# Performance work log

Hardware: AMD Instinct MI355X
Metric: run time of the kernel (lower is better)

Reference implementation:

```python
import jax, jax.numpy as jnp
import numpy as np

B, S, D_MODEL, D_K, D_V = 8, 2048, 1024, 1024, 1024


def setup_inputs() -> dict:
    key = jax.random.key(0)
    ks = jax.random.split(key, 10)
    scale = 1.0 / np.sqrt(D_MODEL)
    return {
        "inputs_q": jax.random.normal(ks[0], (B, S, D_MODEL), dtype=jnp.float32),
        "inputs_k": jax.random.normal(ks[1], (B, S, D_MODEL), dtype=jnp.float32),
        "inputs_v": jax.random.normal(ks[2], (B, S, D_MODEL), dtype=jnp.float32),
        "mask": jax.random.randint(ks[3], (B, S), 0, 2, dtype=jnp.int32),
        "Wq": jax.random.normal(ks[4], (D_MODEL, D_K), dtype=jnp.float32) * scale,
        "bq": jnp.zeros((D_K,), dtype=jnp.float32),
        "Wk": jax.random.normal(ks[5], (D_MODEL, D_K), dtype=jnp.float32) * scale,
        "bk": jnp.zeros((D_K,), dtype=jnp.float32),
        "Wv": jax.random.normal(ks[6], (D_MODEL, D_V), dtype=jnp.float32) * scale,
        "bv": jnp.zeros((D_V,), dtype=jnp.float32),
    }


def reference(inputs_q, inputs_k, inputs_v, mask, Wq, bq, Wk, bk, Wv, bv):
    # Dense projections: [B,S,d_model] @ [d_model,d] + bias
    q = jnp.einsum("bsd,dk->bsk", inputs_q, Wq) + bq
    k = jnp.einsum("bsd,dk->bsk", inputs_k, Wk) + bk
    v = jnp.einsum("bsd,dv->bsv", inputs_v, Wv) + bv
    # scaled dot-product scores [B,S,S]
    scores = jnp.einsum("bqk,bsk->bqs", q, k) / jnp.sqrt(jnp.float32(D_K))
    # padding mask [B,S] -> matrix mask via min(row, col); 1 = valid
    m = mask.astype(jnp.float32)
    matrix_mask = jnp.minimum(m[:, :, None], m[:, None, :])  # [B,S,S]
    mask_float = 1.0 - matrix_mask  # 1 where masked
    scores = scores + mask_float * (-1e9)
    attention_weights = jax.nn.softmax(scores, axis=-1)
    out = jnp.einsum("bqs,bsv->bqv", attention_weights, v)  # [B,S,d_v]
    return out
```

## Files before the change

### kernel.cpp

```cpp
#include <hip/hip_runtime.h>
#include <stdint.h>


typedef unsigned short u16;
typedef __attribute__((ext_vector_type(8))) short short8;
typedef __attribute__((ext_vector_type(4))) float f32x4;

__device__ __forceinline__ u16 f2bf(float x) {
  unsigned u = __float_as_uint(x);
  return (u16)((u + 0x7FFFu + ((u >> 16) & 1u)) >> 16);
}
__device__ __forceinline__ float bf2f(u16 h) {
  return __uint_as_float(((unsigned)h) << 16);
}

__device__ __forceinline__ void stage16(const void* g, void* l) {
  const __attribute__((address_space(1))) uint32_t* gp =
      (const __attribute__((address_space(1))) uint32_t*)(uintptr_t)g;
  __attribute__((address_space(3))) uint32_t* lp =
      (__attribute__((address_space(3))) uint32_t*)(uintptr_t)l;
  __builtin_amdgcn_global_load_lds(gp, lp, 16, 0, 0);
}

__device__ __forceinline__ short8 ld8(const char* p, int off) {
  return *(const short8*)(p + off);
}

__global__ __launch_bounds__(256) void maskscan(const int* __restrict__ mask,
                                                int* __restrict__ idxA,
                                                int* __restrict__ nvA,
                                                int* __restrict__ nvpadA) {
  const int b = blockIdx.x;
  const int t = threadIdx.x, lane = t & 63, w = t >> 6;
  const int* m = mask + b * 2048;
  int v[8], loc = 0;
#pragma unroll
  for (int i = 0; i < 8; ++i) { v[i] = m[t * 8 + i]; loc += v[i]; }
  int sc = loc;
  for (int off = 1; off < 64; off <<= 1) {
    int n = __shfl_up(sc, off);
    if (lane >= off) sc += n;
  }
  __shared__ int wsum[4];
  if (lane == 63) wsum[w] = sc;
  __syncthreads();
  int woff = 0;
  for (int i = 0; i < w; ++i) woff += wsum[i];
  int pos = woff + sc - loc;
#pragma unroll
  for (int i = 0; i < 8; ++i)
    if (v[i]) idxA[b * 2048 + (pos++)] = t * 8 + i;
  if (t == 255) {
    const int nv = woff + sc;
    nvA[b] = nv;
    nvpadA[b] = (nv + 255) & ~255;
  }
}

__global__ __launch_bounds__(256) void compact3(const float* __restrict__ Xq,
                                                const float* __restrict__ Xk,
                                                const float* __restrict__ Xv,
                                                const int* __restrict__ idxA,
                                                const int* __restrict__ nvA,
                                                u16* __restrict__ Oq,
                                                u16* __restrict__ Ok,
                                                u16* __restrict__ Ov) {
  const int b = blockIdx.y, j = blockIdx.x, z = blockIdx.z;
  if (j >= nvA[b]) return;
  const float* X = (z == 0) ? Xq : (z == 1) ? Xk : Xv;
  u16* out = (z == 0) ? Oq : (z == 1) ? Ok : Ov;
  const int src = idxA[b * 2048 + j];
  const float4* s = (const float4*)(X + ((size_t)b * 2048 + src) * 1024);
  ushort4* d = (ushort4*)(out + ((size_t)b * 2048 + j) * 1024);
  const float4 f = s[threadIdx.x];
  ushort4 o;
  o.x = f2bf(f.x); o.y = f2bf(f.y); o.z = f2bf(f.z); o.w = f2bf(f.w);
  d[threadIdx.x] = o;
}

__global__ __launch_bounds__(256) void colpart(const float* __restrict__ X,
                                               float* __restrict__ partial) {
  const int b = blockIdx.x, dq = blockIdx.y, sck = blockIdx.z;
  const int d = dq * 256 + threadIdx.x;
  const float* p = X + ((size_t)b * 2048 + sck * 256) * 1024 + d;
  float s0 = 0, s1 = 0, s2 = 0, s3 = 0;
  for (int r = 0; r < 256; r += 4) {
    s0 += p[(size_t)(r + 0) * 1024];
    s1 += p[(size_t)(r + 1) * 1024];
    s2 += p[(size_t)(r + 2) * 1024];
    s3 += p[(size_t)(r + 3) * 1024];
  }
  partial[((size_t)b * 8 + sck) * 1024 + d] = (s0 + s1) + (s2 + s3);
}

__global__ __launch_bounds__(256) void vpartk(const float* __restrict__ partial,
                                              const float* __restrict__ Wv,
                                              float* __restrict__ vpart) {
  const int b = blockIdx.x, cq = blockIdx.y, dk = blockIdx.z;
  const int t = threadIdx.x;
  __shared__ float mx[128];
  if (t < 128) {
    const int d = dk * 128 + t;
    float m = 0;
#pragma unroll
    for (int i = 0; i < 8; ++i) m += partial[((size_t)b * 8 + i) * 1024 + d];
    mx[t] = m * (1.0f / 2048.0f);
  }
  __syncthreads();
  const int c = cq * 256 + t;
  const float* wp = Wv + (size_t)(dk * 128) * 1024 + c;
  float acc = 0;
#pragma unroll 4
  for (int i = 0; i < 128; ++i) acc += mx[i] * wp[(size_t)i * 1024];
  vpart[((size_t)b * 8 + dk) * 1024 + c] = acc;
}

__global__ __launch_bounds__(256) void vmeanred(const float* __restrict__ vpart,
                                                const float* __restrict__ bv,
                                                float* __restrict__ vmean) {
  const int b = blockIdx.x;
  const int c = blockIdx.y * 256 + threadIdx.x;
  float acc = bv[c];
#pragma unroll
  for (int i = 0; i < 8; ++i) acc += vpart[((size_t)b * 8 + i) * 1024 + c];
  vmean[b * 1024 + c] = acc;
}

__global__ __launch_bounds__(256) void bcast(const int* __restrict__ mask,
                                             const float* __restrict__ vmean,
                                             float* __restrict__ out) {
  const int b = blockIdx.y, row = blockIdx.x;
  if (mask[b * 2048 + row] != 0) return;
  const float4 vv = ((const float4*)(vmean + b * 1024))[threadIdx.x];
  ((float4*)(out + ((size_t)b * 2048 + row) * 1024))[threadIdx.x] = vv;
}

__global__ __launch_bounds__(256) void wtrans3(const float* __restrict__ Wq,
                                               const float* __restrict__ Wk,
                                               const float* __restrict__ Wv,
                                               u16* __restrict__ WT) {
  __shared__ float tile[32][33];
  const int z = blockIdx.z;
  const float* W = (z == 0) ? Wq : (z == 1) ? Wk : Wv;
  u16* out = WT + (size_t)z * 1024 * 1024;
  const int tx = threadIdx.x, ty = threadIdx.y;
  const int d0 = blockIdx.y * 32, n0 = blockIdx.x * 32;
#pragma unroll
  for (int i = 0; i < 4; ++i)
    tile[ty + 8 * i][tx] = W[(size_t)(d0 + ty + 8 * i) * 1024 + n0 + tx];
  __syncthreads();
#pragma unroll
  for (int i = 0; i < 4; ++i)
    out[(size_t)(n0 + ty + 8 * i) * 1024 + d0 + tx] = f2bf(tile[tx][ty + 8 * i]);
}


#define BAR __builtin_amdgcn_s_barrier()
#define SB __builtin_amdgcn_sched_barrier(0)
#define LGK0 asm volatile("s_waitcnt lgkmcnt(0)" ::: "memory")
#define VM4 asm volatile("s_waitcnt vmcnt(4)" ::: "memory")
#define VM0 asm volatile("s_waitcnt vmcnt(0)" ::: "memory")

#define RDA4(P0, P1, MH)                                      \
  {                                                           \
    _Pragma("unroll") for (int mf_ = 0; mf_ < 4; ++mf_) {     \
      afr[0][mf_] = ld8(P0, (MH) * 8192 + mf_ * 2048);        \
      afr[1][mf_] = ld8(P1, (MH) * 8192 + mf_ * 2048);        \
    }                                                         \
  }

#define RDB2(DST, P0, P1, NH)                                 \
  {                                                           \
    DST[0][0] = ld8(P0, (NH) * 4096);                         \
    DST[0][1] = ld8(P0, (NH) * 4096 + 2048);                  \
    DST[1][0] = ld8(P1, (NH) * 4096);                         \
    DST[1][1] = ld8(P1, (NH) * 4096 + 2048);                  \
  }

#define MQ16(ACC, NH, BF)                                                \
  __builtin_amdgcn_s_setprio(1);                                         \
  {                                                                      \
    _Pragma("unroll") for (int ks_ = 0; ks_ < 2; ++ks_)                  \
        _Pragma("unroll") for (int mf_ = 0; mf_ < 4; ++mf_)              \
            _Pragma("unroll") for (int nf_ = 0; nf_ < 2; ++nf_)          \
                ACC[mf_][(NH) * 2 + nf_] =                               \
                    __builtin_amdgcn_mfma_f32_16x16x32_bf16(             \
                        afr[ks_][mf_], BF[ks_][nf_],                     \
                        ACC[mf_][(NH) * 2 + nf_], 0, 0, 0);              \
  }                                                                      \
  __builtin_amdgcn_s_setprio(0);

template <int MODE>
__global__ __launch_bounds__(512, 2) void gemm8p(
    const u16* __restrict__ A, const u16* __restrict__ B,
    void* __restrict__ C, void* __restrict__ C1, void* __restrict__ C2,
    const float* __restrict__ b0, const float* __restrict__ b1,
    const float* __restrict__ b2,
    const int* __restrict__ nvpadA, const int* __restrict__ nvA,
    const int* __restrict__ idxA,
    int K, int lda, int ldb, int ldc,
    size_t Az, size_t Bz, size_t Cz) {
  __shared__ __attribute__((aligned(16))) char smem[131072];
  const int tid = threadIdx.x;
  const int lane = tid & 63;
  const int w = tid >> 6;
  const int wr = w >> 2;
  const int wc = w & 3;

  const int bx = blockIdx.x;
  const int z = bx & 7;
  int r = bx >> 3;
  int bm, bn, o = 0;
  if constexpr (MODE == 0) { o = r >> 5; r &= 31; bm = r >> 2; bn = r & 3; }
  else if constexpr (MODE == 2) { bm = r >> 3; bn = r & 7; }
  else { bm = r >> 2; bn = r & 3; }

  const int nvp = nvpadA[z];
  if (bm * 256 >= nvp) return;
  if constexpr (MODE == 2) { if (bn * 256 >= nvp) return; }

  const u16* Ap = A;
  const u16* Bp = B;
  if constexpr (MODE == 0) {
    Ap += (size_t)o * (8u * 2048u * 1024u) + (size_t)z * (2048u * 1024u);
    Bp += (size_t)o * (1024u * 1024u);
  } else {
    Ap += (size_t)z * Az;
    Bp += (size_t)z * Bz;
  }
  const int Kz = (MODE == 3) ? nvp : K;
  const int half = Kz >> 7;

  const int srow = w * 8 + (lane >> 3);
  const int scol = ((lane & 7) ^ (lane >> 3)) << 3;
  const u16* Ab0 = Ap + (size_t)(bm * 256 + srow) * lda + scol;
  const u16* Ab1 = Ab0 + (size_t)64 * lda;
  const u16* Ab2 = Ab0 + (size_t)128 * lda;
  const u16* Ab3 = Ab0 + (size_t)192 * lda;
  const u16* Bb0 = Bp + (size_t)(bn * 256 + srow) * ldb + scol;
  const u16* Bb1 = Bb0 + (size_t)64 * ldb;
  const u16* Bb2 = Bb0 + (size_t)128 * ldb;
  const u16* Bb3 = Bb0 + (size_t)192 * ldb;
  char* ldsW = smem + w * 1024;

  const int fr = lane & 15;
  const int fq = lane >> 4;
  const int fx = (fr & 7) << 4;
  const char* pak0 = smem + wr * 16384 + fr * 128 + ((fq * 16) ^ fx);
  const char* pak1 = smem + wr * 16384 + fr * 128 + ((64 + fq * 16) ^ fx);
  const char* pak0b = pak0 + 65536;
  const char* pak1b = pak1 + 65536;
  const char* pbk0 = smem + 32768 + wc * 8192 + fr * 128 + ((fq * 16) ^ fx);
  const char* pbk1 = smem + 32768 + wc * 8192 + fr * 128 + ((64 + fq * 16) ^ fx);
  const char* pbk0b = pbk0 + 65536;
  const char* pbk1b = pbk1 + 65536;

  f32x4 acc0[4][4] = {};
  f32x4 acc1[4][4] = {};
  short8 afr[2][4], bf0[2][2], bf1[2][2];

  stage16(Bb0, ldsW + 32768); stage16(Bb1, ldsW + 40960);
  stage16(Bb2, ldsW + 49152); stage16(Bb3, ldsW + 57344);
  stage16(Ab0, ldsW + 0);     stage16(Ab1, ldsW + 8192);
  stage16(Ab2, ldsW + 16384); stage16(Ab3, ldsW + 24576);
  stage16(Bb0 + 64, ldsW + 98304);  stage16(Bb1 + 64, ldsW + 106496);
  stage16(Bb2 + 64, ldsW + 114688); stage16(Bb3 + 64, ldsW + 122880);
  VM4;
  BAR;

  int koff = 0;
  for (int i = 0; i < half - 1; ++i) {
    const int o1 = koff + 64, o2 = koff + 128, o3 = koff + 192;
    RDA4(pak0, pak1, 0); RDB2(bf0, pbk0, pbk1, 0);
    stage16(Ab0 + o1, ldsW + 65536); stage16(Ab1 + o1, ldsW + 73728);
    SB; BAR; LGK0; MQ16(acc0, 0, bf0); BAR;
    RDB2(bf1, pbk0, pbk1, 1);
    stage16(Ab2 + o1, ldsW + 81920); stage16(Ab3 + o1, ldsW + 90112);
    SB; BAR; LGK0; MQ16(acc0, 1, bf1); BAR;
    RDA4(pak0, pak1, 1);
    stage16(Bb0 + o2, ldsW + 32768); stage16(Bb1 + o2, ldsW + 40960);
    SB; BAR; LGK0; MQ16(acc1, 0, bf0); BAR;
    stage16(Bb2 + o2, ldsW + 49152); stage16(Bb3 + o2, ldsW + 57344);
    SB; BAR; MQ16(acc1, 1, bf1); VM4; BAR;
    RDA4(pak0b, pak1b, 0); RDB2(bf0, pbk0b, pbk1b, 0);
    stage16(Ab0 + o2, ldsW + 0); stage16(Ab1 + o2, ldsW + 8192);
    SB; BAR; LGK0; MQ16(acc0, 0, bf0); BAR;
    RDB2(bf1, pbk0b, pbk1b, 1);
    stage16(Ab2 + o2, ldsW + 16384); stage16(Ab3 + o2, ldsW + 24576);
    SB; BAR; LGK0; MQ16(acc0, 1, bf1); BAR;
    RDA4(pak0b, pak1b, 1);
    stage16(Bb0 + o3, ldsW + 98304); stage16(Bb1 + o3, ldsW + 106496);
    SB; BAR; LGK0; MQ16(acc1, 0, bf0); BAR;
    stage16(Bb2 + o3, ldsW + 114688); stage16(Bb3 + o3, ldsW + 122880);
    SB; BAR; MQ16(acc1, 1, bf1); VM4; BAR;
    koff += 128;
  }
  {
    const int o1 = koff + 64;
    RDA4(pak0, pak1, 0); RDB2(bf0, pbk0, pbk1, 0);
    stage16(Ab0 + o1, ldsW + 65536); stage16(Ab1 + o1, ldsW + 73728);
    SB; BAR; LGK0; MQ16(acc0, 0, bf0); BAR;
    RDB2(bf1, pbk0, pbk1, 1);
    stage16(Ab2 + o1, ldsW + 81920); stage16(Ab3 + o1, ldsW + 90112);
    SB; BAR; LGK0; MQ16(acc0, 1, bf1); BAR;
    RDA4(pak0, pak1, 1);
    SB; BAR; LGK0; MQ16(acc1, 0, bf0); BAR;
    SB; BAR; MQ16(acc1, 1, bf1); VM0; BAR;
    RDA4(pak0b, pak1b, 0); RDB2(bf0, pbk0b, pbk1b, 0);
    SB; BAR; LGK0; MQ16(acc0, 0, bf0); BAR;
    RDB2(bf1, pbk0b, pbk1b, 1);
    SB; BAR; LGK0; MQ16(acc0, 1, bf1); BAR;
    RDA4(pak0b, pak1b, 1);
    SB; BAR; LGK0; MQ16(acc1, 0, bf0); BAR;
    SB; BAR; MQ16(acc1, 1, bf1); BAR;
  }

  const int colb = bn * 256 + wc * 64 + fr;
#pragma unroll
  for (int mh = 0; mh < 2; ++mh) {
    f32x4(&ac)[4][4] = mh ? acc1 : acc0;
    const int rowl = bm * 256 + wr * 128 + mh * 64 + fq * 4;
    if constexpr (MODE == 0) {
      if (o < 2) {
        const float* bp = o ? b1 : b0;
        u16* Cb = (u16*)(o ? C1 : C) + (size_t)z * (2048u * 1024u);
#pragma unroll
        for (int mf = 0; mf < 4; ++mf)
#pragma unroll
          for (int n = 0; n < 4; ++n) {
            const int c = colb + n * 16;
            const float bv = bp[c];
#pragma unroll
            for (int j = 0; j < 4; ++j)
              Cb[(size_t)(rowl + mf * 16 + j) * 1024 + c] =
                  f2bf(ac[mf][n][j] + bv);
          }
      } else {
        u16* Cb = (u16*)C2;
#pragma unroll
        for (int mf = 0; mf < 4; ++mf) {
          const int s_ = rowl + mf * 16;
#pragma unroll
          for (int n = 0; n < 4; ++n) {
            const int c = colb + n * 16;
            const float bv = b2[c];
            ushort4 ov;
            ov.x = f2bf(ac[mf][n][0] + bv);
            ov.y = f2bf(ac[mf][n][1] + bv);
            ov.z = f2bf(ac[mf][n][2] + bv);
            ov.w = f2bf(ac[mf][n][3] + bv);
            *(ushort4*)&Cb[((size_t)z * 1024 + c) * 2048 + s_] = ov;
          }
        }
      }
    } else if constexpr (MODE == 2) {
      u16* Cb = (u16*)C + (size_t)z * Cz;
#pragma unroll
      for (int mf = 0; mf < 4; ++mf)
#pragma unroll
        for (int n = 0; n < 4; ++n) {
          const int c = colb + n * 16;
#pragma unroll
          for (int j = 0; j < 4; ++j)
            Cb[(size_t)(rowl + mf * 16 + j) * ldc + c] =
                f2bf(ac[mf][n][j] * 0.03125f);
        }
    } else {
      const int nv = nvA[z];
      const int* idxp = idxA + z * 2048;
      float* Ob = (float*)C;
#pragma unroll
      for (int mf = 0; mf < 4; ++mf)
#pragma unroll
        for (int j = 0; j < 4; ++j) {
          const int rowc = rowl + mf * 16 + j;
          if (rowc < nv) {
            const int gr = idxp[rowc];
            float* orow = Ob + ((size_t)z * 2048 + gr) * 1024;
#pragma unroll
            for (int n = 0; n < 4; ++n) orow[colb + n * 16] = ac[mf][n][j];
          }
        }
    }
  }
}

__global__ __launch_bounds__(256) void softmaxc(u16* __restrict__ scores,
                                                const int* __restrict__ nvA,
                                                const int* __restrict__ nvpadA) {
  const int b = blockIdx.y, row = blockIdx.x;
  const int nv = nvA[b];
  if (row >= nv) return;
  const int nvp = nvpadA[b];
  const int t = threadIdx.x, lane = t & 63, w = t >> 6;
  u16* sc = scores + ((size_t)b * 2048 + row) * 2048;
  const int c0 = t * 8;
  float v[8];
  if (c0 < nvp) {
    const ushort4 h0 = *(const ushort4*)&sc[c0];
    const ushort4 h1 = *(const ushort4*)&sc[c0 + 4];
    v[0] = bf2f(h0.x); v[1] = bf2f(h0.y); v[2] = bf2f(h0.z); v[3] = bf2f(h0.w);
    v[4] = bf2f(h1.x); v[5] = bf2f(h1.y); v[6] = bf2f(h1.z); v[7] = bf2f(h1.w);
  } else {
#pragma unroll
    for (int i = 0; i < 8; ++i) v[i] = 0.f;
  }
  float lmax = -3.0e38f;
#pragma unroll
  for (int i = 0; i < 8; ++i)
    if (c0 + i < nv) lmax = fmaxf(lmax, v[i]);
#pragma unroll
  for (int off = 32; off >= 1; off >>= 1) lmax = fmaxf(lmax, __shfl_xor(lmax, off));
  __shared__ float red[8];
  if (lane == 0) red[w] = lmax;
  __syncthreads();
  const float bmax = fmaxf(fmaxf(red[0], red[1]), fmaxf(red[2], red[3]));
  float e[8];
  float lsum = 0.f;
#pragma unroll
  for (int i = 0; i < 8; ++i) {
    e[i] = (c0 + i < nv) ? __expf(v[i] - bmax) : 0.f;
    lsum += e[i];
  }
#pragma unroll
  for (int off = 32; off >= 1; off >>= 1) lsum += __shfl_xor(lsum, off);
  if (lane == 0) red[4 + w] = lsum;
  __syncthreads();
  const float inv = 1.0f / ((red[4] + red[5]) + (red[6] + red[7]));
  if (c0 < nvp) {
    ushort4 o0, o1;
    o0.x = f2bf(e[0] * inv); o0.y = f2bf(e[1] * inv);
    o0.z = f2bf(e[2] * inv); o0.w = f2bf(e[3] * inv);
    o1.x = f2bf(e[4] * inv); o1.y = f2bf(e[5] * inv);
    o1.z = f2bf(e[6] * inv); o1.w = f2bf(e[7] * inv);
    *(ushort4*)&sc[c0] = o0;
    *(ushort4*)&sc[c0 + 4] = o1;
  }
}

extern "C" void kernel_launch(void* const* d_in, const int* in_sizes, int n_in,
                              void* d_out, int out_size, void* d_ws, size_t ws_size,
                              hipStream_t stream) {
  const float* in_q = (const float*)d_in[0];
  const float* in_k = (const float*)d_in[1];
  const float* in_v = (const float*)d_in[2];
  const int* mask = (const int*)d_in[3];
  const float* Wq = (const float*)d_in[4];
  const float* bq = (const float*)d_in[5];
  const float* Wk = (const float*)d_in[6];
  const float* bk = (const float*)d_in[7];
  const float* Wv = (const float*)d_in[8];
  const float* bv = (const float*)d_in[9];

  char* ws = (char*)d_ws;
  const size_t SZ = (size_t)16384 * 1024 * 2;
  u16* qc = (u16*)(ws);
  u16* kc = (u16*)(ws + SZ);
  u16* vcT = (u16*)(ws + 2 * SZ);
  u16* Xc = (u16*)(ws + 3 * SZ);
  u16* Xqc = Xc;
  u16* Xkc = Xc + (size_t)8 * 2048 * 1024;
  u16* Xvc = Xkc + (size_t)8 * 2048 * 1024;
  u16* scores = (u16*)(ws + 3 * SZ);
  u16* WT = (u16*)(ws + 6 * SZ);
  char* misc = ws + 6 * SZ + 6 * 1024 * 1024;
  int* idxA = (int*)misc;
  int* nvA = idxA + 8 * 2048;
  int* nvpadA = nvA + 8;
  float* partial = (float*)(misc + 128 * 1024);
  float* vmean = (float*)(misc + 384 * 1024);
  float* vpart = (float*)(misc + 448 * 1024);

  maskscan<<<8, 256, 0, stream>>>(mask, idxA, nvA, nvpadA);

  compact3<<<dim3(2048, 8, 3), 256, 0, stream>>>(in_q, in_k, in_v, idxA, nvA,
                                                 Xqc, Xkc, Xvc);
  colpart<<<dim3(8, 4, 8), 256, 0, stream>>>(in_v, partial);
  vpartk<<<dim3(8, 4, 8), 256, 0, stream>>>(partial, Wv, vpart);
  vmeanred<<<dim3(8, 4), 256, 0, stream>>>(vpart, bv, vmean);

  wtrans3<<<dim3(32, 32, 3), dim3(32, 8), 0, stream>>>(Wq, Wk, Wv, WT);

  gemm8p<0><<<768, 512, 0, stream>>>(
      Xqc, WT, qc, kc, vcT, bq, bk, bv, nvpadA, nvA, idxA,
      1024, 1024, 1024, 1024, 0, 0, 0);

  gemm8p<2><<<512, 512, 0, stream>>>(
      qc, kc, scores, nullptr, nullptr, nullptr, nullptr, nullptr,
      nvpadA, nvA, idxA, 1024, 1024, 1024, 2048,
      (size_t)2048 * 1024, (size_t)2048 * 1024, (size_t)2048 * 2048);

  softmaxc<<<dim3(2048, 8), 256, 0, stream>>>(scores, nvA, nvpadA);

  gemm8p<3><<<256, 512, 0, stream>>>(
      scores, vcT, d_out, nullptr, nullptr, nullptr, nullptr, nullptr,
      nvpadA, nvA, idxA, 0, 2048, 2048, 1024,
      (size_t)2048 * 2048, (size_t)1024 * 2048, 0);

  bcast<<<dim3(2048, 8), 256, 0, stream>>>(mask, vmean, (float*)d_out);
}
```

Measured before the change: 282.5 us.

## Use 128-tile simple GEMM for scores and PV with 128-row padding

Replaces the 256x256 pipelined gemm8p kernel for the QK^T and attention-times-V stages with a new simple 128x128-tile kernel (gemm128). The valid-length padding drops from a multiple of 256 to a multiple of 128, which cuts wasted compute on padded rows, columns and K. The new kernel is single-buffered, stages through global_load_lds, and syncs twice per 32-wide K step, so it gives up the software pipelining and larger-tile reuse of the old path. gemm8p is reduced to the projection mode only.

```diff
diff --git a/kernel.cpp b/kernel.cpp
--- a/kernel.cpp
+++ b/kernel.cpp
@@ -29,7 +29,8 @@
 __global__ __launch_bounds__(256) void maskscan(const int* __restrict__ mask,
                                                 int* __restrict__ idxA,
                                                 int* __restrict__ nvA,
-                                                int* __restrict__ nvpadA) {
+                                                int* __restrict__ nvpadA,
+                                                int* __restrict__ nvp128A) {
   const int b = blockIdx.x;
   const int t = threadIdx.x, lane = t & 63, w = t >> 6;
   const int* m = mask + b * 2048;
@@ -54,6 +55,7 @@
     const int nv = woff + sc;
     nvA[b] = nv;
     nvpadA[b] = (nv + 255) & ~255;
+    nvp128A[b] = (nv + 127) & ~127;
   }
 }
 
@@ -154,7 +156,6 @@
     out[(size_t)(n0 + ty + 8 * i) * 1024 + d0 + tx] = f2bf(tile[tx][ty + 8 * i]);
 }
 
-
 #define BAR __builtin_amdgcn_s_barrier()
 #define SB __builtin_amdgcn_sched_barrier(0)
 #define LGK0 asm volatile("s_waitcnt lgkmcnt(0)" ::: "memory")
@@ -196,10 +197,8 @@
     void* __restrict__ C, void* __restrict__ C1, void* __restrict__ C2,
     const float* __restrict__ b0, const float* __restrict__ b1,
     const float* __restrict__ b2,
-    const int* __restrict__ nvpadA, const int* __restrict__ nvA,
-    const int* __restrict__ idxA,
-    int K, int lda, int ldb, int ldc,
-    size_t Az, size_t Bz, size_t Cz) {
+    const int* __restrict__ nvpadA,
+    int K, int lda, int ldb, int ldc) {
   __shared__ __attribute__((aligned(16))) char smem[131072];
   const int tid = threadIdx.x;
   const int lane = tid & 63;
@@ -210,26 +209,15 @@
   const int bx = blockIdx.x;
   const int z = bx & 7;
   int r = bx >> 3;
-  int bm, bn, o = 0;
-  if constexpr (MODE == 0) { o = r >> 5; r &= 31; bm = r >> 2; bn = r & 3; }
-  else if constexpr (MODE == 2) { bm = r >> 3; bn = r & 7; }
-  else { bm = r >> 2; bn = r & 3; }
+  const int o = r >> 5; r &= 31;
+  const int bm = r >> 2, bn = r & 3;
 
   const int nvp = nvpadA[z];
   if (bm * 256 >= nvp) return;
-  if constexpr (MODE == 2) { if (bn * 256 >= nvp) return; }
-
-  const u16* Ap = A;
-  const u16* Bp = B;
-  if constexpr (MODE == 0) {
-    Ap += (size_t)o * (8u * 2048u * 1024u) + (size_t)z * (2048u * 1024u);
-    Bp += (size_t)o * (1024u * 1024u);
-  } else {
-    Ap += (size_t)z * Az;
-    Bp += (size_t)z * Bz;
-  }
-  const int Kz = (MODE == 3) ? nvp : K;
-  const int half = Kz >> 7;
+
+  const u16* Ap = A + (size_t)o * (8u * 2048u * 1024u) + (size_t)z * (2048u * 1024u);
+  const u16* Bp = B + (size_t)o * (1024u * 1024u);
+  const int half = K >> 7;
 
   const int srow = w * 8 + (lane >> 3);
   const int scol = ((lane & 7) ^ (lane >> 3)) << 3;
@@ -320,78 +308,149 @@
   for (int mh = 0; mh < 2; ++mh) {
     f32x4(&ac)[4][4] = mh ? acc1 : acc0;
     const int rowl = bm * 256 + wr * 128 + mh * 64 + fq * 4;
-    if constexpr (MODE == 0) {
-      if (o < 2) {
-        const float* bp = o ? b1 : b0;
-        u16* Cb = (u16*)(o ? C1 : C) + (size_t)z * (2048u * 1024u);
-#pragma unroll
-        for (int mf = 0; mf < 4; ++mf)
-#pragma unroll
-          for (int n = 0; n < 4; ++n) {
-            const int c = colb + n * 16;
-            const float bv = bp[c];
-#pragma unroll
-            for (int j = 0; j < 4; ++j)
-              Cb[(size_t)(rowl + mf * 16 + j) * 1024 + c] =
-                  f2bf(ac[mf][n][j] + bv);
-          }
-      } else {
-        u16* Cb = (u16*)C2;
-#pragma unroll
-        for (int mf = 0; mf < 4; ++mf) {
-          const int s_ = rowl + mf * 16;
-#pragma unroll
-          for (int n = 0; n < 4; ++n) {
-            const int c = colb + n * 16;
-            const float bv = b2[c];
-            ushort4 ov;
-            ov.x = f2bf(ac[mf][n][0] + bv);
-            ov.y = f2bf(ac[mf][n][1] + bv);
-            ov.z = f2bf(ac[mf][n][2] + bv);
-            ov.w = f2bf(ac[mf][n][3] + bv);
-            *(ushort4*)&Cb[((size_t)z * 1024 + c) * 2048 + s_] = ov;
-          }
+    if (o < 2) {
+      const float* bp = o ? b1 : b0;
+      u16* Cb = (u16*)(o ? C1 : C) + (size_t)z * (2048u * 1024u);
+#pragma unroll
+      for (int mf = 0; mf < 4; ++mf)
+#pragma unroll
+        for (int n = 0; n < 4; ++n) {
+          const int c = colb + n * 16;
+          const float bv = bp[c];
+#pragma unroll
+          for (int j = 0; j < 4; ++j)
+            Cb[(size_t)(rowl + mf * 16 + j) * ldc + c] = f2bf(ac[mf][n][j] + bv);
+        }
+    } else {
+      u16* Cb = (u16*)C2;
+#pragma unroll
+      for (int mf = 0; mf < 4; ++mf) {
+        const int s_ = rowl + mf * 16;
+#pragma unroll
+        for (int n = 0; n < 4; ++n) {
+          const int c = colb + n * 16;
+          const float bv = b2[c];
+          ushort4 ov;
+          ov.x = f2bf(ac[mf][n][0] + bv);
+          ov.y = f2bf(ac[mf][n][1] + bv);
+          ov.z = f2bf(ac[mf][n][2] + bv);
+          ov.w = f2bf(ac[mf][n][3] + bv);
+          *(ushort4*)&Cb[((size_t)z * 1024 + c) * 2048 + s_] = ov;
         }
       }
-    } else if constexpr (MODE == 2) {
-      u16* Cb = (u16*)C + (size_t)z * Cz;
-#pragma unroll
-      for (int mf = 0; mf < 4; ++mf)
-#pragma unroll
-        for (int n = 0; n < 4; ++n) {
-          const int c = colb + n * 16;
-#pragma unroll
-          for (int j = 0; j < 4; ++j)
-            Cb[(size_t)(rowl + mf * 16 + j) * ldc + c] =
-                f2bf(ac[mf][n][j] * 0.03125f);
+    }
+  }
+}
+
+template <int MODE>
+__global__ __launch_bounds__(256, 2) void gemm128(
+    const u16* __restrict__ A, const u16* __restrict__ B, void* __restrict__ C,
+    const int* __restrict__ nvp128A, const int* __restrict__ nvA,
+    const int* __restrict__ idxA,
+    int K, int lda, int ldb, int ldc,
+    size_t Az, size_t Bz, size_t Cz) {
+  __shared__ __attribute__((aligned(16))) u16 lsA[128 * 32];
+  __shared__ __attribute__((aligned(16))) u16 lsB[128 * 32];
+  const int tid = threadIdx.x;
+  const int lane = tid & 63;
+  const int w = tid >> 6;
+  const int wr = w >> 1, wc = w & 1;
+
+  const int bx = blockIdx.x;
+  const int z = bx & 7;
+  const int r = bx >> 3;
+  int bm, bn;
+  if constexpr (MODE == 2) { bm = r >> 4; bn = r & 15; }
+  else                     { bm = r >> 3; bn = r & 7; }
+
+  const int nvp = nvp128A[z];
+  if (bm * 128 >= nvp) return;
+  if constexpr (MODE == 2) { if (bn * 128 >= nvp) return; }
+  const int Kz = (MODE == 3) ? nvp : K;
+
+  const u16* Ap = A + (size_t)z * Az;
+  const u16* Bp = B + (size_t)z * Bz;
+
+  const int srow = lane >> 2;
+  const int scol = (lane & 3) * 8;
+  const u16* Ag0 = Ap + (size_t)(bm * 128 + w * 32 + srow) * lda + scol;
+  const u16* Ag1 = Ag0 + (size_t)16 * lda;
+  const u16* Bg0 = Bp + (size_t)(bn * 128 + w * 32 + srow) * ldb + scol;
+  const u16* Bg1 = Bg0 + (size_t)16 * ldb;
+  u16* lA0 = &lsA[(w * 32) * 32];
+  u16* lA1 = &lsA[(w * 32 + 16) * 32];
+  u16* lB0 = &lsB[(w * 32) * 32];
+  u16* lB1 = &lsB[(w * 32 + 16) * 32];
+
+  const int arow = wr * 64 + (lane & 15);
+  const int brow = wc * 64 + (lane & 15);
+  const int ko = (lane >> 4) * 8;
+
+  f32x4 acc[4][4] = {};
+
+  for (int k0 = 0; k0 < Kz; k0 += 32) {
+    stage16(Ag0 + k0, lA0);
+    stage16(Ag1 + k0, lA1);
+    stage16(Bg0 + k0, lB0);
+    stage16(Bg1 + k0, lB1);
+    __syncthreads();
+    short8 af[4], bfr[4];
+#pragma unroll
+    for (int m = 0; m < 4; ++m)
+      af[m] = *(const short8*)&lsA[(arow + m * 16) * 32 + ko];
+#pragma unroll
+    for (int n = 0; n < 4; ++n)
+      bfr[n] = *(const short8*)&lsB[(brow + n * 16) * 32 + ko];
+#pragma unroll
+    for (int m = 0; m < 4; ++m)
+#pragma unroll
+      for (int n = 0; n < 4; ++n)
+        acc[m][n] =
+            __builtin_amdgcn_mfma_f32_16x16x32_bf16(af[m], bfr[n], acc[m][n], 0, 0, 0);
+    __syncthreads();
+  }
+
+  const int col0 = bn * 128 + wc * 64 + (lane & 15);
+  const int row0 = bm * 128 + wr * 64 + ((lane >> 4) << 2);
+
+  if constexpr (MODE == 2) {
+    u16* Cb = (u16*)C + (size_t)z * Cz;
+#pragma unroll
+    for (int m = 0; m < 4; ++m)
+#pragma unroll
+      for (int n = 0; n < 4; ++n) {
+        const int c = col0 + n * 16;
+#pragma unroll
+        for (int j = 0; j < 4; ++j)
+          Cb[(size_t)(row0 + m * 16 + j) * ldc + c] =
+              f2bf(acc[m][n][j] * 0.03125f);
+      }
+  } else {
+    const int nv = nvA[z];
+    const int* idxp = idxA + z * 2048;
+    float* Ob = (float*)C;
+#pragma unroll
+    for (int m = 0; m < 4; ++m)
+#pragma unroll
+      for (int j = 0; j < 4; ++j) {
+        const int rowc = row0 + m * 16 + j;
+        if (rowc < nv) {
+          const int gr = idxp[rowc];
+          float* orow = Ob + ((size_t)z * 2048 + gr) * 1024;
+#pragma unroll
+          for (int n = 0; n < 4; ++n) orow[col0 + n * 16] = acc[m][n][j];
         }
-    } else {
-      const int nv = nvA[z];
-      const int* idxp = idxA + z * 2048;
-      float* Ob = (float*)C;
-#pragma unroll
-      for (int mf = 0; mf < 4; ++mf)
-#pragma unroll
-        for (int j = 0; j < 4; ++j) {
-          const int rowc = rowl + mf * 16 + j;
-          if (rowc < nv) {
-            const int gr = idxp[rowc];
-            float* orow = Ob + ((size_t)z * 2048 + gr) * 1024;
-#pragma unroll
-            for (int n = 0; n < 4; ++n) orow[colb + n * 16] = ac[mf][n][j];
-          }
-        }
-    }
+      }
   }
 }
 
 __global__ __launch_bounds__(256) void softmaxc(u16* __restrict__ scores,
                                                 const int* __restrict__ nvA,
-                                                const int* __restrict__ nvpadA) {
+                                                const int* __restrict__ nvp128A) {
   const int b = blockIdx.y, row = blockIdx.x;
   const int nv = nvA[b];
   if (row >= nv) return;
-  const int nvp = nvpadA[b];
+  const int nvp = nvp128A[b];
   const int t = threadIdx.x, lane = t & 63, w = t >> 6;
   u16* sc = scores + ((size_t)b * 2048 + row) * 2048;
   const int c0 = t * 8;
@@ -467,11 +526,12 @@
   int* idxA = (int*)misc;
   int* nvA = idxA + 8 * 2048;
   int* nvpadA = nvA + 8;
+  int* nvp128A = nvpadA + 8;
   float* partial = (float*)(misc + 128 * 1024);
   float* vmean = (float*)(misc + 384 * 1024);
   float* vpart = (float*)(misc + 448 * 1024);
 
-  maskscan<<<8, 256, 0, stream>>>(mask, idxA, nvA, nvpadA);
+  maskscan<<<8, 256, 0, stream>>>(mask, idxA, nvA, nvpadA, nvp128A);
 
   compact3<<<dim3(2048, 8, 3), 256, 0, stream>>>(in_q, in_k, in_v, idxA, nvA,
                                                  Xqc, Xkc, Xvc);
@@ -482,19 +542,16 @@
   wtrans3<<<dim3(32, 32, 3), dim3(32, 8), 0, stream>>>(Wq, Wk, Wv, WT);
 
   gemm8p<0><<<768, 512, 0, stream>>>(
-      Xqc, WT, qc, kc, vcT, bq, bk, bv, nvpadA, nvA, idxA,
-      1024, 1024, 1024, 1024, 0, 0, 0);
-
-  gemm8p<2><<<512, 512, 0, stream>>>(
-      qc, kc, scores, nullptr, nullptr, nullptr, nullptr, nullptr,
-      nvpadA, nvA, idxA, 1024, 1024, 1024, 2048,
+      Xqc, WT, qc, kc, vcT, bq, bk, bv, nvpadA, 1024, 1024, 1024, 1024);
+
+  gemm128<2><<<2048, 256, 0, stream>>>(
+      qc, kc, scores, nvp128A, nvA, idxA, 1024, 1024, 1024, 2048,
       (size_t)2048 * 1024, (size_t)2048 * 1024, (size_t)2048 * 2048);
 
-  softmaxc<<<dim3(2048, 8), 256, 0, stream>>>(scores, nvA, nvpadA);
-
-  gemm8p<3><<<256, 512, 0, stream>>>(
-      scores, vcT, d_out, nullptr, nullptr, nullptr, nullptr, nullptr,
-      nvpadA, nvA, idxA, 0, 2048, 2048, 1024,
+  softmaxc<<<dim3(2048, 8), 256, 0, stream>>>(scores, nvA, nvp128A);
+
+  gemm128<3><<<1024, 256, 0, stream>>>(
+      scores, vcT, d_out, nvp128A, nvA, idxA, 0, 2048, 2048, 1024,
       (size_t)2048 * 2048, (size_t)1024 * 2048, 0);
 
   bcast<<<dim3(2048, 8), 256, 0, stream>>>(mask, vmean, (float*)d_out);
```

Measured after the change: 255.7 us. -9.5%, faster.
